# Performance work log

Measured on AMD Instinct MI355X. Metric: run time of the kernel, lower is better.

The kernel has to match this reference:

```python
import jax, jax.numpy as jnp
import numpy as np


def setup_inputs() -> dict:
    key = jax.random.key(0)
    k1, k2, k3, k4 = jax.random.split(key, 4)
    B, S, H = 32768, 128, 64
    origins = jax.random.normal(k1, (B, 3), dtype=jnp.float32)
    directions = jax.random.normal(k2, (B, 3), dtype=jnp.float32)
    W1 = jax.random.normal(k3, (3, H), dtype=jnp.float32) * 0.5
    b1 = jnp.zeros((H,), dtype=jnp.float32)
    W2 = jax.random.normal(k4, (H, 4), dtype=jnp.float32) * 0.1
    b2 = jnp.zeros((4,), dtype=jnp.float32)
    return {
        "origins": origins,
        "directions": directions,
        "near": jnp.float32(2.0),
        "far": jnp.float32(6.0),
        "W1": W1,
        "b1": b1,
        "W2": W2,
        "b2": b2,
        "num_samples": S,
    }


def reference(origins, directions, near, far, W1, b1, W2, b2, num_samples):
    B = origins.shape[0]
    S = num_samples
    # segment boundaries [S+1] and midpoints [S] along each ray
    t = jnp.linspace(0.0, 1.0, S + 1, dtype=origins.dtype)
    boundaries = near + (far - near) * t                      # [S+1]
    mids = 0.5 * (boundaries[1:] + boundaries[:-1])           # [S]
    # normalized directions (F.normalize with eps clamp on norm)
    norm = jnp.linalg.norm(directions, axis=-1, keepdims=True)
    d = directions / jnp.maximum(norm, 1e-12)                 # [B,3]
    # sample locations [B,S,3]
    samples = origins[:, None, :] + mids[None, :, None] * d[:, None, :]
    # field: 2-layer ReLU MLP, exp-mapped outputs
    x = samples.reshape(-1, 3)                                # [B*S,3]
    h = jax.nn.relu(x @ W1 + b1)                              # [B*S,H]
    field_values = jnp.exp(h @ W2 + b2)                       # [B*S,4]
    sigmas = field_values[:, -1].reshape(B, S)                # [B,S]
    colors = field_values[:, :-1].reshape(B, S, 3)            # [B,S,3]
    # alpha values from densities and segment lengths
    deltas = boundaries[1:] - boundaries[:-1]                 # [S]
    alphas = 1.0 - jnp.exp(-sigmas * deltas[None, :])         # [B,S]
    # alpha compositing (inclusive cumprod, as in the source)
    T = jnp.cumprod(1.0 - alphas, axis=-1)                    # [B,S]
    w = T * alphas                                            # [B,S]
    return jnp.einsum("bs,bsc->bc", w, colors)                # [B,3]
```

## Files before the change

kernel.cpp:

```cpp
#include <hip/hip_runtime.h>


constexpr int S_TOTAL = 128;
constexpr int TPR     = 8;
constexpr int SPT     = S_TOTAL / TPR;
constexpr int BLOCK   = 256;
constexpr int H       = 64;

__global__ __launch_bounds__(BLOCK, 4)
void nerf_fused(const float* __restrict__ origins,
                const float* __restrict__ directions,
                const float* __restrict__ nearp,
                const float* __restrict__ farp,
                const float* __restrict__ W1,
                const float* __restrict__ b1,
                const float* __restrict__ W2,
                const float* __restrict__ b2,
                float* __restrict__ out,
                int B)
{
    __shared__ float pk[H][8];
    __shared__ float b2s[4];

    const int tid = threadIdx.x;
    if (tid < H) {
        pk[tid][0] = W1[0 * H + tid];
        pk[tid][1] = W1[1 * H + tid];
        pk[tid][2] = W1[2 * H + tid];
        pk[tid][3] = b1[tid];
        pk[tid][4] = W2[tid * 4 + 0];
        pk[tid][5] = W2[tid * 4 + 1];
        pk[tid][6] = W2[tid * 4 + 2];
        pk[tid][7] = W2[tid * 4 + 3];
    }
    if (tid < 4) b2s[tid] = b2[tid];
    __syncthreads();

    const int gtid = blockIdx.x * BLOCK + tid;
    const int ray  = gtid >> 3;
    const int sub  = gtid & (TPR - 1);
    if (ray >= B) return;

    const float o0 = origins[ray * 3 + 0];
    const float o1 = origins[ray * 3 + 1];
    const float o2 = origins[ray * 3 + 2];
    float d0 = directions[ray * 3 + 0];
    float d1 = directions[ray * 3 + 1];
    float d2 = directions[ray * 3 + 2];

    const float nr    = nearp[0];
    const float fr    = farp[0];
    const float delta = (fr - nr) * (1.0f / (float)S_TOTAL);

    const float nrm  = sqrtf(d0 * d0 + d1 * d1 + d2 * d2);
    const float rinv = 1.0f / fmaxf(nrm, 1e-12f);
    d0 *= rinv; d1 *= rinv; d2 *= rinv;

    float m[SPT];
#pragma unroll
    for (int k = 0; k < SPT; ++k)
        m[k] = fmaf((float)(sub * SPT + k) + 0.5f, delta, nr);

    const float b20 = b2s[0], b21 = b2s[1], b22 = b2s[2], b23 = b2s[3];
    float4 acc[SPT];
#pragma unroll
    for (int k = 0; k < SPT; ++k) acc[k] = make_float4(b20, b21, b22, b23);

#pragma unroll 4
    for (int h = 0; h < H; ++h) {
        const float4 pa = *reinterpret_cast<const float4*>(&pk[h][0]);
        const float4 pb = *reinterpret_cast<const float4*>(&pk[h][4]);
        const float Ah = fmaf(o2, pa.z, fmaf(o1, pa.y, fmaf(o0, pa.x, pa.w)));
        const float Bh = fmaf(d2, pa.z, fmaf(d1, pa.y, d0 * pa.x));
#pragma unroll
        for (int k = 0; k < SPT; ++k) {
            const float hv = fmaxf(fmaf(m[k], Bh, Ah), 0.0f);
            acc[k].x = fmaf(hv, pb.x, acc[k].x);
            acc[k].y = fmaf(hv, pb.y, acc[k].y);
            acc[k].z = fmaf(hv, pb.z, acc[k].z);
            acc[k].w = fmaf(hv, pb.w, acc[k].w);
        }
    }

    float Tloc = 1.0f, orr = 0.0f, og = 0.0f, ob = 0.0f;
#pragma unroll
    for (int k = 0; k < SPT; ++k) {
        const float sig = __expf(acc[k].w);
        const float e   = __expf(-sig * delta);
        Tloc *= e;
        const float w = Tloc * (1.0f - e);
        orr = fmaf(w, __expf(acc[k].x), orr);
        og  = fmaf(w, __expf(acc[k].y), og);
        ob  = fmaf(w, __expf(acc[k].z), ob);
    }

    float scan = Tloc;
#pragma unroll
    for (int off = 1; off < TPR; off <<= 1) {
        const float v = __shfl_up(scan, off, TPR);
        if (sub >= off) scan *= v;
    }
    float pre = __shfl_up(scan, 1, TPR);
    if (sub == 0) pre = 1.0f;

    orr *= pre; og *= pre; ob *= pre;
#pragma unroll
    for (int off = TPR / 2; off > 0; off >>= 1) {
        orr += __shfl_down(orr, off, TPR);
        og  += __shfl_down(og,  off, TPR);
        ob  += __shfl_down(ob,  off, TPR);
    }

    if (sub == 0) {
        out[ray * 3 + 0] = orr;
        out[ray * 3 + 1] = og;
        out[ray * 3 + 2] = ob;
    }
}

extern "C" void kernel_launch(void* const* d_in, const int* in_sizes, int n_in,
                              void* d_out, int out_size, void* d_ws, size_t ws_size,
                              hipStream_t stream) {
    const float* origins    = (const float*)d_in[0];
    const float* directions = (const float*)d_in[1];
    const float* nearp      = (const float*)d_in[2];
    const float* farp       = (const float*)d_in[3];
    const float* W1         = (const float*)d_in[4];
    const float* b1         = (const float*)d_in[5];
    const float* W2         = (const float*)d_in[6];
    const float* b2         = (const float*)d_in[7];
    float* out              = (float*)d_out;

    const int B     = in_sizes[0] / 3;
    const int total = B * TPR;
    const int grid  = (total + BLOCK - 1) / BLOCK;

    nerf_fused<<<grid, BLOCK, 0, stream>>>(origins, directions, nearp, farp,
                                           W1, b1, W2, b2, out, B);
}
```

Measured before the change: 42.83 us.

## Precompute per-ray hidden-layer affine terms in shared memory, use 16 threads per ray

Raises threads per ray from 8 to 16, halving samples per thread, and doubles the occupancy hint in launch bounds. The per-hidden-unit affine terms A_h and B_h for each ray are now computed once per block into shared memory and no longer recomputed redundantly by every thread of the ray. This cuts inner-loop ALU work and register pressure in exchange for a larger shared footprint, a cooperative precompute phase, and a longer scan/reduction across 16 lanes. The early bounds check on the ray index was removed, so the kernel relies on B being a multiple of rays per block.

```diff
diff --git a/kernel.cpp b/kernel.cpp
--- a/kernel.cpp
+++ b/kernel.cpp
@@ -2,12 +2,13 @@
 
 
 constexpr int S_TOTAL = 128;
-constexpr int TPR     = 8;
+constexpr int TPR     = 16;
 constexpr int SPT     = S_TOTAL / TPR;
 constexpr int BLOCK   = 256;
+constexpr int RPB     = BLOCK / TPR;
 constexpr int H       = 64;
 
-__global__ __launch_bounds__(BLOCK, 4)
+__global__ __launch_bounds__(BLOCK, 8)
 void nerf_fused(const float* __restrict__ origins,
                 const float* __restrict__ directions,
                 const float* __restrict__ nearp,
@@ -19,42 +20,50 @@
                 float* __restrict__ out,
                 int B)
 {
-    __shared__ float pk[H][8];
+    __shared__ float ABs[RPB][H + 1][2];
+    __shared__ float W2s[H][4];
     __shared__ float b2s[4];
 
-    const int tid = threadIdx.x;
+    const int tid  = threadIdx.x;
+    const int ray0 = blockIdx.x * RPB;
+
     if (tid < H) {
-        pk[tid][0] = W1[0 * H + tid];
-        pk[tid][1] = W1[1 * H + tid];
-        pk[tid][2] = W1[2 * H + tid];
-        pk[tid][3] = b1[tid];
-        pk[tid][4] = W2[tid * 4 + 0];
-        pk[tid][5] = W2[tid * 4 + 1];
-        pk[tid][6] = W2[tid * 4 + 2];
-        pk[tid][7] = W2[tid * 4 + 3];
+        W2s[tid][0] = W2[tid * 4 + 0];
+        W2s[tid][1] = W2[tid * 4 + 1];
+        W2s[tid][2] = W2[tid * 4 + 2];
+        W2s[tid][3] = W2[tid * 4 + 3];
     }
     if (tid < 4) b2s[tid] = b2[tid];
+
+#pragma unroll
+    for (int idx = tid; idx < RPB * H; idx += BLOCK) {
+        const int r   = idx >> 6;
+        const int h   = idx & (H - 1);
+        const int ray = ray0 + r;
+        const float o0 = origins[ray * 3 + 0];
+        const float o1 = origins[ray * 3 + 1];
+        const float o2 = origins[ray * 3 + 2];
+        float d0 = directions[ray * 3 + 0];
+        float d1 = directions[ray * 3 + 1];
+        float d2 = directions[ray * 3 + 2];
+        const float nrm  = sqrtf(d0 * d0 + d1 * d1 + d2 * d2);
+        const float rinv = 1.0f / fmaxf(nrm, 1e-12f);
+        d0 *= rinv; d1 *= rinv; d2 *= rinv;
+        const float w0 = W1[0 * H + h];
+        const float w1 = W1[1 * H + h];
+        const float w2 = W1[2 * H + h];
+        ABs[r][h][0] = fmaf(o2, w2, fmaf(o1, w1, fmaf(o0, w0, b1[h])));
+        ABs[r][h][1] = fmaf(d2, w2, fmaf(d1, w1, d0 * w0));
+    }
     __syncthreads();
 
-    const int gtid = blockIdx.x * BLOCK + tid;
-    const int ray  = gtid >> 3;
-    const int sub  = gtid & (TPR - 1);
-    if (ray >= B) return;
-
-    const float o0 = origins[ray * 3 + 0];
-    const float o1 = origins[ray * 3 + 1];
-    const float o2 = origins[ray * 3 + 2];
-    float d0 = directions[ray * 3 + 0];
-    float d1 = directions[ray * 3 + 1];
-    float d2 = directions[ray * 3 + 2];
+    const int sub  = tid & (TPR - 1);
+    const int rloc = tid >> 4;
+    const int ray  = ray0 + rloc;
 
     const float nr    = nearp[0];
     const float fr    = farp[0];
     const float delta = (fr - nr) * (1.0f / (float)S_TOTAL);
-
-    const float nrm  = sqrtf(d0 * d0 + d1 * d1 + d2 * d2);
-    const float rinv = 1.0f / fmaxf(nrm, 1e-12f);
-    d0 *= rinv; d1 *= rinv; d2 *= rinv;
 
     float m[SPT];
 #pragma unroll
@@ -68,13 +77,11 @@
 
 #pragma unroll 4
     for (int h = 0; h < H; ++h) {
-        const float4 pa = *reinterpret_cast<const float4*>(&pk[h][0]);
-        const float4 pb = *reinterpret_cast<const float4*>(&pk[h][4]);
-        const float Ah = fmaf(o2, pa.z, fmaf(o1, pa.y, fmaf(o0, pa.x, pa.w)));
-        const float Bh = fmaf(d2, pa.z, fmaf(d1, pa.y, d0 * pa.x));
+        const float2 ab = *reinterpret_cast<const float2*>(&ABs[rloc][h][0]);
+        const float4 pb = *reinterpret_cast<const float4*>(&W2s[h][0]);
 #pragma unroll
         for (int k = 0; k < SPT; ++k) {
-            const float hv = fmaxf(fmaf(m[k], Bh, Ah), 0.0f);
+            const float hv = fmaxf(fmaf(m[k], ab.y, ab.x), 0.0f);
             acc[k].x = fmaf(hv, pb.x, acc[k].x);
             acc[k].y = fmaf(hv, pb.y, acc[k].y);
             acc[k].z = fmaf(hv, pb.z, acc[k].z);
```

Result: faster. 40.69 us (-5.0%).

## Replace per-sample MLP with piecewise-linear difference-array prefix scan

Applied to the files above, without the earlier changes.

Along each ray the preactivation of every hidden unit is linear in sample position, so each ReLU turns on or off at a single crossing index. Each hidden unit now adds its W2-weighted A and B coefficients into a shared-memory difference array at that crossing. A prefix scan across 32 threads per ray then gives the layer-2 outputs as affine functions of t. This turns the O(S·H) inner loop into O(H) atomics plus an O(S) scan, at the cost of shared-memory atomics, a large per-block LDS footprint, and possible rounding mismatches at boundary samples.

```diff
diff --git a/kernel.cpp b/kernel.cpp
--- a/kernel.cpp
+++ b/kernel.cpp
@@ -2,116 +2,160 @@
 
 
 constexpr int S_TOTAL = 128;
-constexpr int TPR     = 8;
+constexpr int TPR     = 32;
 constexpr int SPT     = S_TOTAL / TPR;
 constexpr int BLOCK   = 256;
+constexpr int RPB     = BLOCK / TPR;
 constexpr int H       = 64;
+constexpr int SLOTS   = 132;
 
 __global__ __launch_bounds__(BLOCK, 4)
-void nerf_fused(const float* __restrict__ origins,
-                const float* __restrict__ directions,
-                const float* __restrict__ nearp,
-                const float* __restrict__ farp,
-                const float* __restrict__ W1,
-                const float* __restrict__ b1,
-                const float* __restrict__ W2,
-                const float* __restrict__ b2,
-                float* __restrict__ out,
-                int B)
+void nerf_scan(const float* __restrict__ origins,
+               const float* __restrict__ directions,
+               const float* __restrict__ nearp,
+               const float* __restrict__ farp,
+               const float* __restrict__ W1,
+               const float* __restrict__ b1,
+               const float* __restrict__ W2,
+               const float* __restrict__ b2,
+               float* __restrict__ out,
+               int B)
 {
-    __shared__ float pk[H][8];
-    __shared__ float b2s[4];
+    __shared__ float dif[RPB][8][SLOTS];
 
     const int tid = threadIdx.x;
-    if (tid < H) {
-        pk[tid][0] = W1[0 * H + tid];
-        pk[tid][1] = W1[1 * H + tid];
-        pk[tid][2] = W1[2 * H + tid];
-        pk[tid][3] = b1[tid];
-        pk[tid][4] = W2[tid * 4 + 0];
-        pk[tid][5] = W2[tid * 4 + 1];
-        pk[tid][6] = W2[tid * 4 + 2];
-        pk[tid][7] = W2[tid * 4 + 3];
+    {
+        float* p = &dif[0][0][0];
+        for (int i = tid; i < RPB * 8 * SLOTS; i += BLOCK) p[i] = 0.0f;
     }
-    if (tid < 4) b2s[tid] = b2[tid];
     __syncthreads();
 
-    const int gtid = blockIdx.x * BLOCK + tid;
-    const int ray  = gtid >> 3;
-    const int sub  = gtid & (TPR - 1);
-    if (ray >= B) return;
-
-    const float o0 = origins[ray * 3 + 0];
-    const float o1 = origins[ray * 3 + 1];
-    const float o2 = origins[ray * 3 + 2];
-    float d0 = directions[ray * 3 + 0];
-    float d1 = directions[ray * 3 + 1];
-    float d2 = directions[ray * 3 + 2];
+    const int rloc = tid >> 5;
+    const int sub  = tid & 31;
+    const int ray  = blockIdx.x * RPB + rloc;
+    const int rayc = (ray < B) ? ray : (B - 1);
 
     const float nr    = nearp[0];
     const float fr    = farp[0];
     const float delta = (fr - nr) * (1.0f / (float)S_TOTAL);
 
+    const float o0 = origins[rayc * 3 + 0];
+    const float o1 = origins[rayc * 3 + 1];
+    const float o2 = origins[rayc * 3 + 2];
+    float d0 = directions[rayc * 3 + 0];
+    float d1 = directions[rayc * 3 + 1];
+    float d2 = directions[rayc * 3 + 2];
     const float nrm  = sqrtf(d0 * d0 + d1 * d1 + d2 * d2);
     const float rinv = 1.0f / fmaxf(nrm, 1e-12f);
     d0 *= rinv; d1 *= rinv; d2 *= rinv;
 
-    float m[SPT];
+    float* const dp = &dif[rloc][0][0];
+
+#define ATOM8(IDX, SGN)                                                       \
+    {                                                                         \
+        const int _i = (IDX);                                                 \
+        atomicAdd(dp + 0 * SLOTS + _i, SGN wa0);                              \
+        atomicAdd(dp + 1 * SLOTS + _i, SGN wa1);                              \
+        atomicAdd(dp + 2 * SLOTS + _i, SGN wa2);                              \
+        atomicAdd(dp + 3 * SLOTS + _i, SGN wa3);                              \
+        atomicAdd(dp + 4 * SLOTS + _i, SGN wb0);                              \
+        atomicAdd(dp + 5 * SLOTS + _i, SGN wb1);                              \
+        atomicAdd(dp + 6 * SLOTS + _i, SGN wb2);                              \
+        atomicAdd(dp + 7 * SLOTS + _i, SGN wb3);                              \
+    }
+
 #pragma unroll
-    for (int k = 0; k < SPT; ++k)
-        m[k] = fmaf((float)(sub * SPT + k) + 0.5f, delta, nr);
+    for (int hh = 0; hh < 2; ++hh) {
+        const int h = sub + 32 * hh;
+        const float u0 = W1[0 * H + h];
+        const float u1 = W1[1 * H + h];
+        const float u2 = W1[2 * H + h];
+        const float A  = fmaf(o2, u2, fmaf(o1, u1, fmaf(o0, u0, b1[h])));
+        const float Bc = fmaf(d2, u2, fmaf(d1, u1, d0 * u0));
+        const float C0    = fmaf(nr + 0.5f * delta, Bc, A);
+        const float slope = delta * Bc;
 
-    const float b20 = b2s[0], b21 = b2s[1], b22 = b2s[2], b23 = b2s[3];
-    float4 acc[SPT];
-#pragma unroll
-    for (int k = 0; k < SPT; ++k) acc[k] = make_float4(b20, b21, b22, b23);
+        const float wa0 = W2[h * 4 + 0] * A,  wa1 = W2[h * 4 + 1] * A;
+        const float wa2 = W2[h * 4 + 2] * A,  wa3 = W2[h * 4 + 3] * A;
+        const float wb0 = W2[h * 4 + 0] * Bc, wb1 = W2[h * 4 + 1] * Bc;
+        const float wb2 = W2[h * 4 + 2] * Bc, wb3 = W2[h * 4 + 3] * Bc;
 
-#pragma unroll 4
-    for (int h = 0; h < H; ++h) {
-        const float4 pa = *reinterpret_cast<const float4*>(&pk[h][0]);
-        const float4 pb = *reinterpret_cast<const float4*>(&pk[h][4]);
-        const float Ah = fmaf(o2, pa.z, fmaf(o1, pa.y, fmaf(o0, pa.x, pa.w)));
-        const float Bh = fmaf(d2, pa.z, fmaf(d1, pa.y, d0 * pa.x));
-#pragma unroll
-        for (int k = 0; k < SPT; ++k) {
-            const float hv = fmaxf(fmaf(m[k], Bh, Ah), 0.0f);
-            acc[k].x = fmaf(hv, pb.x, acc[k].x);
-            acc[k].y = fmaf(hv, pb.y, acc[k].y);
-            acc[k].z = fmaf(hv, pb.z, acc[k].z);
-            acc[k].w = fmaf(hv, pb.w, acc[k].w);
+        if (slope > 0.0f) {
+            const float sc = -C0 / slope;
+            const int lo = (sc < 0.0f) ? 0 : ((int)floorf(sc) + 1);
+            if (lo < S_TOTAL) ATOM8(lo, +)
+        } else if (slope < 0.0f) {
+            const float sc = -C0 / slope;
+            if (sc > 0.0f) {
+                ATOM8(0, +)
+                const int hi = (int)ceilf(sc);
+                if (hi < S_TOTAL) ATOM8(hi, -)
+            }
+        } else {
+            if (C0 > 0.0f) ATOM8(0, +)
         }
     }
+#undef ATOM8
+    __syncthreads();
 
+    const int s0 = sub * SPT;
+    float p[8][SPT];
+#pragma unroll
+    for (int c = 0; c < 8; ++c) {
+        const float4 v = *reinterpret_cast<const float4*>(&dif[rloc][c][s0]);
+        float v0 = v.x, v1 = v.y, v2 = v.z, v3 = v.w;
+        v1 += v0; v2 += v1; v3 += v2;
+        p[c][0] = v0; p[c][1] = v1; p[c][2] = v2; p[c][3] = v3;
+    }
+#pragma unroll
+    for (int c = 0; c < 8; ++c) {
+        float t = p[c][3];
+#pragma unroll
+        for (int off = 1; off < 32; off <<= 1) {
+            const float u = __shfl_up(t, off, 32);
+            if (sub >= off) t += u;
+        }
+        float ex = __shfl_up(t, 1, 32);
+        ex = (sub == 0) ? 0.0f : ex;
+        p[c][0] += ex; p[c][1] += ex; p[c][2] += ex; p[c][3] += ex;
+    }
+
+    const float b20 = b2[0], b21 = b2[1], b22 = b2[2], b23 = b2[3];
     float Tloc = 1.0f, orr = 0.0f, og = 0.0f, ob = 0.0f;
 #pragma unroll
     for (int k = 0; k < SPT; ++k) {
-        const float sig = __expf(acc[k].w);
+        const float m  = fmaf((float)(s0 + k) + 0.5f, delta, nr);
+        const float c0 = b20 + fmaf(m, p[4][k], p[0][k]);
+        const float c1 = b21 + fmaf(m, p[5][k], p[1][k]);
+        const float c2 = b22 + fmaf(m, p[6][k], p[2][k]);
+        const float sg = b23 + fmaf(m, p[7][k], p[3][k]);
+        const float sig = __expf(sg);
         const float e   = __expf(-sig * delta);
         Tloc *= e;
         const float w = Tloc * (1.0f - e);
-        orr = fmaf(w, __expf(acc[k].x), orr);
-        og  = fmaf(w, __expf(acc[k].y), og);
-        ob  = fmaf(w, __expf(acc[k].z), ob);
+        orr = fmaf(w, __expf(c0), orr);
+        og  = fmaf(w, __expf(c1), og);
+        ob  = fmaf(w, __expf(c2), ob);
     }
 
     float scan = Tloc;
 #pragma unroll
-    for (int off = 1; off < TPR; off <<= 1) {
-        const float v = __shfl_up(scan, off, TPR);
+    for (int off = 1; off < 32; off <<= 1) {
+        const float v = __shfl_up(scan, off, 32);
         if (sub >= off) scan *= v;
     }
-    float pre = __shfl_up(scan, 1, TPR);
+    float pre = __shfl_up(scan, 1, 32);
     if (sub == 0) pre = 1.0f;
 
     orr *= pre; og *= pre; ob *= pre;
 #pragma unroll
-    for (int off = TPR / 2; off > 0; off >>= 1) {
-        orr += __shfl_down(orr, off, TPR);
-        og  += __shfl_down(og,  off, TPR);
-        ob  += __shfl_down(ob,  off, TPR);
+    for (int off = 16; off > 0; off >>= 1) {
+        orr += __shfl_down(orr, off, 32);
+        og  += __shfl_down(og,  off, 32);
+        ob  += __shfl_down(ob,  off, 32);
     }
 
-    if (sub == 0) {
+    if (sub == 0 && ray < B) {
         out[ray * 3 + 0] = orr;
         out[ray * 3 + 1] = og;
         out[ray * 3 + 2] = ob;
@@ -131,10 +175,9 @@
     const float* b2         = (const float*)d_in[7];
     float* out              = (float*)d_out;
 
-    const int B     = in_sizes[0] / 3;
-    const int total = B * TPR;
-    const int grid  = (total + BLOCK - 1) / BLOCK;
+    const int B    = in_sizes[0] / 3;
+    const int grid = (B + RPB - 1) / RPB;
 
-    nerf_fused<<<grid, BLOCK, 0, stream>>>(origins, directions, nearp, farp,
-                                           W1, b1, W2, b2, out, B);
+    nerf_scan<<<grid, BLOCK, 0, stream>>>(origins, directions, nearp, farp,
+                                          W1, b1, W2, b2, out, B);
 }
```

Result: slower. 88.19 us (+105.9%).
